# Optimization experiments

Hardware: AMD Instinct MI355X
Metric: run time of the kernel (lower is better)

Reference implementation:

```python
import jax, jax.numpy as jnp
import numpy as np


def setup_inputs() -> dict:
    key = jax.random.key(0)
    k1, k2 = jax.random.split(key)
    B, N, M = 8, 8192, 8192
    pred = jax.random.normal(k1, (B, N, 3), dtype=jnp.float32)
    gt = jax.random.normal(k2, (B, M, 3), dtype=jnp.float32)
    return {"pred": pred, "gt": gt}


def _chamfer(pred, gt):
    # pred: [B,N,3], gt: [B,M,3]
    # squared pairwise distances: ||p||^2 + ||q||^2 - 2 p.q  -> [B,N,M]
    p_sq = jnp.sum(pred * pred, axis=-1)           # [B,N]
    q_sq = jnp.sum(gt * gt, axis=-1)               # [B,M]
    cross = jnp.einsum('bnd,bmd->bnm', pred, gt)   # [B,N,M]
    dist = p_sq[:, :, None] + q_sq[:, None, :] - 2.0 * cross
    dist = jnp.maximum(dist, 0.0)  # numerical floor, distances are non-negative
    # kaolin chamfer_distance: mean over points of nearest-neighbor sq-dist, both sides
    p2q = jnp.mean(jnp.min(dist, axis=2), axis=1)  # [B]
    q2p = jnp.mean(jnp.min(dist, axis=1), axis=1)  # [B]
    chamfer = p2q + q2p                            # [B] (w1 = w2 = 1)
    return jnp.mean(chamfer)                       # scalar, torch.mean over batch


def reference(pred, gt):
    return _chamfer(pred, gt)
```

## Files before the change

kernel.cpp:

```cpp
#include <hip/hip_runtime.h>


typedef short bf16x8 __attribute__((ext_vector_type(8)));
typedef float f32x16 __attribute__((ext_vector_type(16)));

#define B_SZ   8
#define NPTS   8192
#define TOTAL  (B_SZ * NPTS)
#define BLOCK  256
#define QB     256
#define SLICE  1024
#define NSTAGE (NPTS / SLICE)
#define TILES  (SLICE / 32)

__device__ __forceinline__ unsigned short bf16rn(float f, float* rem) {
    unsigned u = __float_as_uint(f);
    unsigned h = (u + 0x8000u) & 0xFFFF0000u;
    *rem = f - __uint_as_float(h);
    return (unsigned short)(h >> 16);
}

__global__ __launch_bounds__(BLOCK) void chamfer_prep_mfma(
    const float* __restrict__ gt, const float* __restrict__ pred,
    uint4* __restrict__ TgA, uint4* __restrict__ TgB, float* __restrict__ Wg,
    uint4* __restrict__ TpA, uint4* __restrict__ TpB, float* __restrict__ Wp)
{
    int i = blockIdx.x * BLOCK + threadIdx.x;
    const float* src = blockIdx.y ? pred : gt;
    uint4* TA = blockIdx.y ? TpA : TgA;
    uint4* TB = blockIdx.y ? TpB : TgB;
    float* W  = blockIdx.y ? Wp  : Wg;

    float x = src[3 * (size_t)i + 0];
    float y = src[3 * (size_t)i + 1];
    float z = src[3 * (size_t)i + 2];
    float w = fmaf(x, x, fmaf(y, y, z * z));
    W[i] = w;

    float ux = -2.f * x, uy = -2.f * y, uz = -2.f * z;
    float rx, ry, rz, dx, dy, dz, rw1, rw2, rw3;
    unsigned short uhx = bf16rn(ux, &rx), uhy = bf16rn(uy, &ry), uhz = bf16rn(uz, &rz);
    unsigned short ulx = bf16rn(rx, &dx), uly = bf16rn(ry, &dy), ulz = bf16rn(rz, &dz);
    unsigned short wh = bf16rn(w, &rw1), wm = bf16rn(rw1, &rw2), wl = bf16rn(rw2, &rw3);
    union { unsigned short s[16]; uint4 v[2]; } A;
    A.s[0] = uhx; A.s[1] = uhy; A.s[2]  = uhz;
    A.s[3] = uhx; A.s[4] = uhy; A.s[5]  = uhz;
    A.s[6] = ulx; A.s[7] = uly; A.s[8]  = ulz;
    A.s[9] = ulx; A.s[10] = uly; A.s[11] = ulz;
    A.s[12] = wh; A.s[13] = wm; A.s[14] = wl; A.s[15] = 0;
    TA[2 * (size_t)i]     = A.v[0];
    TA[2 * (size_t)i + 1] = A.v[1];

    float sx, sy, sz, ex, ey, ez;
    unsigned short qhx = bf16rn(x, &sx), qhy = bf16rn(y, &sy), qhz = bf16rn(z, &sz);
    unsigned short qlx = bf16rn(sx, &ex), qly = bf16rn(sy, &ey), qlz = bf16rn(sz, &ez);
    union { unsigned short s[16]; uint4 v[2]; } Bb;
    Bb.s[0] = qhx; Bb.s[1] = qhy; Bb.s[2]  = qhz;
    Bb.s[3] = qlx; Bb.s[4] = qly; Bb.s[5]  = qlz;
    Bb.s[6] = qhx; Bb.s[7] = qhy; Bb.s[8]  = qhz;
    Bb.s[9] = qlx; Bb.s[10] = qly; Bb.s[11] = qlz;
    Bb.s[12] = 0x3F80; Bb.s[13] = 0x3F80; Bb.s[14] = 0x3F80; Bb.s[15] = 0;
    TB[2 * (size_t)i]     = Bb.v[0];
    TB[2 * (size_t)i + 1] = Bb.v[1];
}

__device__ __forceinline__ void gload_lds16(const void* g, void* l) {
    __builtin_amdgcn_global_load_lds(
        (const __attribute__((address_space(1))) unsigned int*)g,
        (__attribute__((address_space(3))) unsigned int*)l, 16, 0, 0);
}

__device__ __forceinline__ f32x16 min16(f32x16 m, f32x16 d) {
#pragma unroll
    for (int j = 0; j < 16; ++j) m[j] = fminf(m[j], d[j]);
    return m;
}

__device__ __forceinline__ float mintree(f32x16 m) {
    float r0 = fminf(fminf(m[0], m[1]), m[2]);
    float r1 = fminf(fminf(m[3], m[4]), m[5]);
    float r2 = fminf(fminf(m[6], m[7]), m[8]);
    float r3 = fminf(fminf(m[9], m[10]), m[11]);
    float r4 = fminf(fminf(m[12], m[13]), m[14]);
    float s0 = fminf(fminf(r0, r1), r2);
    float s1 = fminf(fminf(r3, r4), m[15]);
    return fminf(s0, s1);
}

__global__ __launch_bounds__(BLOCK, 2) void chamfer_nn_fused(
    const uint4* __restrict__ TgA, const uint4* __restrict__ TpB,
    const float* __restrict__ Wp,
    const uint4* __restrict__ TpA, const uint4* __restrict__ TgB,
    const float* __restrict__ Wg,
    float* __restrict__ out)
{
    __shared__ uint4 tileU[2 * SLICE * 2];
    __shared__ float psum[4];
    char* tileC = (char*)tileU;

    const int qb = blockIdx.x, b = blockIdx.y, dir = blockIdx.z;
    const int t = threadIdx.x, lane = t & 63, wid = t >> 6;
    const int col = lane & 31, hi = lane >> 5;

    const uint4* TA = dir ? TpA : TgA;
    const uint4* TB = dir ? TgB : TpB;
    const float* WQ = dir ? Wg  : Wp;

    const int qblk = qb * QB + wid * 64;
    const char* TBc = (const char*)(TB + ((size_t)b * NPTS + qblk) * 2);
    bf16x8 bq0 = *(const bf16x8*)(TBc + (size_t)col * 32 + hi * 16);
    bf16x8 bq1 = *(const bf16x8*)(TBc + (size_t)(col + 32) * 32 + hi * 16);

    f32x16 zacc;
#pragma unroll
    for (int j = 0; j < 16; ++j) zacc[j] = 0.f;
    f32x16 macc0 = zacc + 3.0e38f;
    f32x16 macc1 = macc0;
    const int abase = (col * 32 + hi * 16) ^ (((col >> 2) & 7) << 4);

    const uint4* TAb = TA + (size_t)b * NPTS * 2;
    const int swzlane = lane ^ (lane >> 3);
    const uint4* gsrc0 = TAb + wid * 512 + swzlane;
    char* ldst0 = tileC + wid * 8192;

#pragma unroll
    for (int it = 0; it < 8; ++it)
        gload_lds16(gsrc0 + it * 64, ldst0 + it * 1024);
    __syncthreads();

    for (int st = 0; st < NSTAGE; ++st) {
        const int cur = (st & 1) << 15;
        if (st + 1 < NSTAGE) {
            const uint4* gs = gsrc0 + (size_t)(st + 1) * (SLICE * 2);
            char* ld = ldst0 + (cur ^ 32768);
#pragma unroll
            for (int it = 0; it < 8; ++it)
                gload_lds16(gs + it * 64, ld + it * 1024);
        }

        const char* tb = tileC + cur + abase;
        bf16x8 a_cur = *(const bf16x8*)(tb);
#pragma unroll 2
        for (int tt = 0; tt < TILES - 1; ++tt) {
            bf16x8 a_nxt = *(const bf16x8*)(tb + (tt + 1) * 1024);
            f32x16 d0 = __builtin_amdgcn_mfma_f32_32x32x16_bf16(a_cur, bq0, zacc, 0, 0, 0);
            f32x16 d1 = __builtin_amdgcn_mfma_f32_32x32x16_bf16(a_cur, bq1, zacc, 0, 0, 0);
            macc0 = min16(macc0, d0);
            macc1 = min16(macc1, d1);
            a_cur = a_nxt;
        }
        f32x16 d0 = __builtin_amdgcn_mfma_f32_32x32x16_bf16(a_cur, bq0, zacc, 0, 0, 0);
        f32x16 d1 = __builtin_amdgcn_mfma_f32_32x32x16_bf16(a_cur, bq1, zacc, 0, 0, 0);
        macc0 = min16(macc0, d0);
        macc1 = min16(macc1, d1);

        __syncthreads();
    }

    float m0 = mintree(macc0);
    float m1 = mintree(macc1);
    m0 = fminf(m0, __shfl_xor(m0, 32));
    m1 = fminf(m1, __shfl_xor(m1, 32));
    float wq = WQ[(size_t)b * NPTS + qb * QB + t];
    float d = fmaxf((lane < 32 ? m0 : m1) + wq, 0.0f);
    float s = d;
#pragma unroll
    for (int o = 1; o < 64; o <<= 1) s += __shfl_xor(s, o);
    if (lane == 0) psum[wid] = s;
    __syncthreads();
    if (t == 0) {
        float tot = (psum[0] + psum[1]) + (psum[2] + psum[3]);
        atomicAdd(out, tot * (1.0f / (float)TOTAL));
    }
}

extern "C" void kernel_launch(void* const* d_in, const int* in_sizes, int n_in,
                              void* d_out, int out_size, void* d_ws, size_t ws_size,
                              hipStream_t stream) {
    const float* pred = (const float*)d_in[0];
    const float* gt   = (const float*)d_in[1];
    float* out = (float*)d_out;

    char* ws = (char*)d_ws;
    uint4* TgA = (uint4*)(ws);
    uint4* TpA = (uint4*)(ws + (size_t)TOTAL * 32);
    uint4* TgB = (uint4*)(ws + (size_t)TOTAL * 64);
    uint4* TpB = (uint4*)(ws + (size_t)TOTAL * 96);
    float* Wg  = (float*)(ws + (size_t)TOTAL * 128);
    float* Wp  = (float*)(ws + (size_t)TOTAL * 128 + (size_t)TOTAL * 4);

    hipMemsetAsync(out, 0, sizeof(float), stream);

    chamfer_prep_mfma<<<dim3(TOTAL / BLOCK, 2), BLOCK, 0, stream>>>(
        gt, pred, TgA, TgB, Wg, TpA, TpB, Wp);

    chamfer_nn_fused<<<dim3(NPTS / QB, B_SZ, 2), BLOCK, 0, stream>>>(
        TgA, TpB, Wp, TpA, TgB, Wg, out);
}
```

Before: 97.69 us.

## Split reference set across blocks with atomicMin merge and separate reduce kernel

Splits the scanned reference points into two halves across extra grid z-blocks, doubling the block count from 512 to 1024 so more CUs stay busy. Per-query minima are combined through atomicMin on float bits in a workspace buffer, and a new reduction kernel sums them. The LDS slice is halved and the launch bounds now ask for 3 blocks per SU. In exchange it adds a memset, atomics and an extra kernel launch. It also adds a dummy third operand to the fmin, which is redundant work unless the compiler folds it.

```diff
diff --git a/kernel.cpp b/kernel.cpp
--- a/kernel.cpp
+++ b/kernel.cpp
@@ -9,9 +9,13 @@
 #define TOTAL  (B_SZ * NPTS)
 #define BLOCK  256
 #define QB     256
-#define SLICE  1024
-#define NSTAGE (NPTS / SLICE)
+#define ZSPLIT 2
+#define HALF   (NPTS / ZSPLIT)
+#define SLICE  512
+#define NSTAGE (HALF / SLICE)
 #define TILES  (SLICE / 32)
+#define BUFB   (SLICE * 32)
+#define RED_GRID 64
 
 __device__ __forceinline__ unsigned short bf16rn(float f, float* rem) {
     unsigned u = __float_as_uint(f);
@@ -70,9 +74,9 @@
         (__attribute__((address_space(3))) unsigned int*)l, 16, 0, 0);
 }
 
-__device__ __forceinline__ f32x16 min16(f32x16 m, f32x16 d) {
-#pragma unroll
-    for (int j = 0; j < 16; ++j) m[j] = fminf(m[j], d[j]);
+__device__ __forceinline__ f32x16 min3x16(f32x16 m, f32x16 d0, f32x16 d1) {
+#pragma unroll
+    for (int j = 0; j < 16; ++j) m[j] = fminf(fminf(m[j], d0[j]), d1[j]);
     return m;
 }
 
@@ -87,24 +91,24 @@
     return fminf(s0, s1);
 }
 
-__global__ __launch_bounds__(BLOCK, 2) void chamfer_nn_fused(
+__global__ __launch_bounds__(BLOCK, 3) void chamfer_nn_mfma(
     const uint4* __restrict__ TgA, const uint4* __restrict__ TpB,
-    const float* __restrict__ Wp,
+    const float* __restrict__ Wp, unsigned* __restrict__ minP,
     const uint4* __restrict__ TpA, const uint4* __restrict__ TgB,
-    const float* __restrict__ Wg,
-    float* __restrict__ out)
+    const float* __restrict__ Wg, unsigned* __restrict__ minG)
 {
     __shared__ uint4 tileU[2 * SLICE * 2];
-    __shared__ float psum[4];
     char* tileC = (char*)tileU;
 
-    const int qb = blockIdx.x, b = blockIdx.y, dir = blockIdx.z;
+    const int qb = blockIdx.x, b = blockIdx.y;
+    const int dir = blockIdx.z >> 1, zs = blockIdx.z & 1;
     const int t = threadIdx.x, lane = t & 63, wid = t >> 6;
     const int col = lane & 31, hi = lane >> 5;
 
     const uint4* TA = dir ? TpA : TgA;
     const uint4* TB = dir ? TgB : TpB;
     const float* WQ = dir ? Wg  : Wp;
+    unsigned*  minb = dir ? minG : minP;
 
     const int qblk = qb * QB + wid * 64;
     const char* TBc = (const char*)(TB + ((size_t)b * NPTS + qblk) * 2);
@@ -118,23 +122,23 @@
     f32x16 macc1 = macc0;
     const int abase = (col * 32 + hi * 16) ^ (((col >> 2) & 7) << 4);
 
-    const uint4* TAb = TA + (size_t)b * NPTS * 2;
+    const uint4* TAb = TA + ((size_t)b * NPTS + (size_t)zs * HALF) * 2;
     const int swzlane = lane ^ (lane >> 3);
-    const uint4* gsrc0 = TAb + wid * 512 + swzlane;
-    char* ldst0 = tileC + wid * 8192;
-
-#pragma unroll
-    for (int it = 0; it < 8; ++it)
+    const uint4* gsrc0 = TAb + wid * 256 + swzlane;
+    char* ldst0 = tileC + wid * 4096;
+
+#pragma unroll
+    for (int it = 0; it < 4; ++it)
         gload_lds16(gsrc0 + it * 64, ldst0 + it * 1024);
     __syncthreads();
 
     for (int st = 0; st < NSTAGE; ++st) {
-        const int cur = (st & 1) << 15;
+        const int cur = (st & 1) * BUFB;
         if (st + 1 < NSTAGE) {
             const uint4* gs = gsrc0 + (size_t)(st + 1) * (SLICE * 2);
-            char* ld = ldst0 + (cur ^ 32768);
-#pragma unroll
-            for (int it = 0; it < 8; ++it)
+            char* ld = ldst0 + (cur ^ BUFB);
+#pragma unroll
+            for (int it = 0; it < 4; ++it)
                 gload_lds16(gs + it * 64, ld + it * 1024);
         }
 
@@ -145,14 +149,14 @@
             bf16x8 a_nxt = *(const bf16x8*)(tb + (tt + 1) * 1024);
             f32x16 d0 = __builtin_amdgcn_mfma_f32_32x32x16_bf16(a_cur, bq0, zacc, 0, 0, 0);
             f32x16 d1 = __builtin_amdgcn_mfma_f32_32x32x16_bf16(a_cur, bq1, zacc, 0, 0, 0);
-            macc0 = min16(macc0, d0);
-            macc1 = min16(macc1, d1);
+            macc0 = min3x16(macc0, d0, zacc + 3.0e38f);
+            macc1 = min3x16(macc1, d1, zacc + 3.0e38f);
             a_cur = a_nxt;
         }
         f32x16 d0 = __builtin_amdgcn_mfma_f32_32x32x16_bf16(a_cur, bq0, zacc, 0, 0, 0);
         f32x16 d1 = __builtin_amdgcn_mfma_f32_32x32x16_bf16(a_cur, bq1, zacc, 0, 0, 0);
-        macc0 = min16(macc0, d0);
-        macc1 = min16(macc1, d1);
+        macc0 = min3x16(macc0, d0, zacc + 3.0e38f);
+        macc1 = min3x16(macc1, d1, zacc + 3.0e38f);
 
         __syncthreads();
     }
@@ -161,16 +165,36 @@
     float m1 = mintree(macc1);
     m0 = fminf(m0, __shfl_xor(m0, 32));
     m1 = fminf(m1, __shfl_xor(m1, 32));
-    float wq = WQ[(size_t)b * NPTS + qb * QB + t];
+    int qi = (int)((size_t)b * NPTS) + qb * QB + t;
+    float wq = WQ[qi];
     float d = fmaxf((lane < 32 ? m0 : m1) + wq, 0.0f);
-    float s = d;
-#pragma unroll
-    for (int o = 1; o < 64; o <<= 1) s += __shfl_xor(s, o);
-    if (lane == 0) psum[wid] = s;
+    atomicMin(&minb[qi], __float_as_uint(d));
+}
+
+__global__ __launch_bounds__(BLOCK) void chamfer_reduce(
+    const float* __restrict__ a, const float* __restrict__ b,
+    float* __restrict__ out, float sc)
+{
+    __shared__ float part[BLOCK / 64];
+    float s = 0.f;
+    int tid = blockIdx.x * BLOCK + threadIdx.x;
+    int stride = gridDim.x * BLOCK;
+    const float4* a4 = (const float4*)a;
+    const float4* b4 = (const float4*)b;
+    for (int i = tid; i < TOTAL / 4; i += stride) {
+        float4 va = a4[i], vb = b4[i];
+        s += (va.x + va.y + va.z + va.w) + (vb.x + vb.y + vb.z + vb.w);
+    }
+    s *= sc;
+    for (int o = 32; o > 0; o >>= 1) s += __shfl_down(s, o, 64);
+    int w = threadIdx.x >> 6;
+    if ((threadIdx.x & 63) == 0) part[w] = s;
     __syncthreads();
-    if (t == 0) {
-        float tot = (psum[0] + psum[1]) + (psum[2] + psum[3]);
-        atomicAdd(out, tot * (1.0f / (float)TOTAL));
+    if (threadIdx.x == 0) {
+        float tot = 0.f;
+#pragma unroll
+        for (int i = 0; i < BLOCK / 64; ++i) tot += part[i];
+        atomicAdd(out, tot);
     }
 }
 
@@ -187,13 +211,19 @@
     uint4* TgB = (uint4*)(ws + (size_t)TOTAL * 64);
     uint4* TpB = (uint4*)(ws + (size_t)TOTAL * 96);
     float* Wg  = (float*)(ws + (size_t)TOTAL * 128);
-    float* Wp  = (float*)(ws + (size_t)TOTAL * 128 + (size_t)TOTAL * 4);
-
+    float* Wp  = (float*)(ws + (size_t)TOTAL * 132);
+    unsigned* minP = (unsigned*)(ws + (size_t)TOTAL * 136);
+    unsigned* minG = (unsigned*)(ws + (size_t)TOTAL * 140);
+
+    hipMemsetAsync(minP, 0x7f, (size_t)TOTAL * 8, stream);
     hipMemsetAsync(out, 0, sizeof(float), stream);
 
     chamfer_prep_mfma<<<dim3(TOTAL / BLOCK, 2), BLOCK, 0, stream>>>(
         gt, pred, TgA, TgB, Wg, TpA, TpB, Wp);
 
-    chamfer_nn_fused<<<dim3(NPTS / QB, B_SZ, 2), BLOCK, 0, stream>>>(
-        TgA, TpB, Wp, TpA, TgB, Wg, out);
-}
+    chamfer_nn_mfma<<<dim3(NPTS / QB, B_SZ, 2 * ZSPLIT), BLOCK, 0, stream>>>(
+        TgA, TpB, Wp, minP, TpA, TgB, Wg, minG);
+
+    chamfer_reduce<<<RED_GRID, BLOCK, 0, stream>>>(
+        (const float*)minP, (const float*)minG, out, 1.0f / (float)TOTAL);
+}
```

After: 108.5 us. 11.1% more time.
